# Kernel optimization log

Measured on AMD Instinct MI355X. Metric: run time of the kernel, lower is better.

Reference implementation:

```python
import jax, jax.numpy as jnp
import numpy as np

NUM_TAGS = 40
SEQ_LEN = 512
BATCH = 2048
INIT_W = 0.57735


def setup_inputs() -> dict:
    key = jax.random.key(0)
    k_em, k_tag, k_tr, k_st, k_en = jax.random.split(key, 5)
    emissions = jax.random.normal(k_em, (SEQ_LEN, BATCH, NUM_TAGS), dtype=jnp.float32)
    tags = jax.random.randint(k_tag, (SEQ_LEN, BATCH), 0, NUM_TAGS, dtype=jnp.int32)
    mask = jnp.ones((SEQ_LEN, BATCH), dtype=bool)
    transitions = jax.random.uniform(k_tr, (NUM_TAGS, NUM_TAGS), minval=-INIT_W, maxval=INIT_W, dtype=jnp.float32)
    start_transitions = jax.random.uniform(k_st, (NUM_TAGS,), minval=-INIT_W, maxval=INIT_W, dtype=jnp.float32)
    end_transitions = jax.random.uniform(k_en, (NUM_TAGS,), minval=-INIT_W, maxval=INIT_W, dtype=jnp.float32)
    return {
        'emissions': emissions,
        'tags': tags,
        'mask': mask,
        'transitions': transitions,
        'start_transitions': start_transitions,
        'end_transitions': end_transitions,
    }


def _seq_score(emissions, tags, mask, transitions, start_transitions, end_transitions):
    # emissions: (L,B,T), tags/mask: (L,B)
    L, B, T = emissions.shape
    maskf = mask.astype(emissions.dtype)
    # emission score of the gold tag at each step: (L,B)
    em = jnp.take_along_axis(emissions, tags[:, :, None].astype(jnp.int32), axis=2)[..., 0]
    score = start_transitions[tags[0]] + em[0]
    # transition + emission for steps 1..L-1, masked
    trans_step = transitions[tags[:-1], tags[1:]]  # (L-1,B)
    score = score + jnp.sum((trans_step + em[1:]) * maskf[1:], axis=0)
    seq_ends = jnp.sum(mask.astype(jnp.int32), axis=0) - 1  # (B,)
    last_tags = tags[seq_ends, jnp.arange(B)]
    score = score + end_transitions[last_tags]
    return score


def _log_normalizer(emissions, mask, transitions, start_transitions, end_transitions):
    # Forward algorithm: sequential scan over time with (B,T) state.
    score0 = start_transitions[None, :] + emissions[0]  # (B,T)

    def step(score, inp):
        em_t, m_t = inp  # (B,T), (B,)
        # broadcast: (B,T_prev,1) + (T_prev,T_next) + (B,1,T_next)
        next_score = jax.nn.logsumexp(score[:, :, None] + transitions[None, :, :] + em_t[:, None, :], axis=1)
        score = jnp.where(m_t[:, None], next_score, score)
        return score, None

    score, _ = jax.lax.scan(step, score0, (emissions[1:], mask[1:]))
    score = score + end_transitions[None, :]
    return jax.nn.logsumexp(score, axis=1)  # (B,)


def reference(emissions, tags, mask, transitions, start_transitions, end_transitions):
    log_num = _seq_score(emissions, tags, mask, transitions, start_transitions, end_transitions)
    log_den = _log_normalizer(emissions, mask, transitions, start_transitions, end_transitions)
    llh = log_num - log_den
    return jnp.sum(llh)  # reduction='sum'
```

## Files before the change

kernel.cpp:

```cpp
#include <hip/hip_runtime.h>

#define L   512
#define B   2048
#define NT  40

#define LOG2E 1.4426950408889634f
#define LN2   0.6931471805599453f

#define EXP2(x) __builtin_amdgcn_exp2f(x)
#define LOG2(x) __builtin_amdgcn_logf(x)

typedef float f32x4  __attribute__((ext_vector_type(4)));
typedef short bf16x8 __attribute__((ext_vector_type(8)));
typedef unsigned int uint4v __attribute__((ext_vector_type(4)));

#define MFMA(a, b, c) __builtin_amdgcn_mfma_f32_16x16x32_bf16(a, b, c, 0, 0, 0)

__device__ __forceinline__ unsigned short bf16_rtn(float x) {
    unsigned int u = __float_as_uint(x);
    u += 0x7FFFu + ((u >> 16) & 1u);
    return (unsigned short)(u >> 16);
}
__device__ __forceinline__ unsigned int cvtpk(float lo, float hi) {
    unsigned int r;
    asm("v_cvt_pk_bf16_f32 %0, %1, %2" : "=v"(r) : "v"(lo), "v"(hi));
    return r;
}
__device__ __forceinline__ float bf2f(short x) {
    return __int_as_float(((int)(unsigned short)x) << 16);
}
__device__ __forceinline__ float bperm_f(int addr, float v) {
    return __int_as_float(__builtin_amdgcn_ds_bpermute(addr, __float_as_int(v)));
}

extern "C" __global__ void __launch_bounds__(128, 2)
crf_main(const float* __restrict__ em, const int* __restrict__ tags,
         const float* __restrict__ trans, const float* __restrict__ st,
         const float* __restrict__ en, float* __restrict__ partial)
{
    __shared__ float sE[NT * NT];
    __shared__ float sT[NT * NT];
    __shared__ float sSt[NT];
    __shared__ float sEn[NT];
    __shared__ float sEn2[NT];
    __shared__ __align__(16) unsigned int sBi[2][16][28];
    __shared__ float sCB[16];
    __shared__ float sNB[16];

    const int tid = threadIdx.x;
    for (int k = tid; k < NT * NT; k += 128) {
        float v = trans[k];
        sT[k] = v;
        sE[k] = __expf(v);
    }
    if (tid < NT) { sSt[tid] = st[tid]; sEn[tid] = en[tid]; sEn2[tid] = en[tid] * LOG2E; }
    __syncthreads();

    const int wave = tid >> 6;
    const int lane = tid & 63;
    const int c    = lane & 15;
    const int g    = lane >> 4;
    const int bc   = blockIdx.x * 16 + c;
    const int i2   = 8 + ((g < 2) ? g : g - 2);
    const int i2s  = (g < 2) ? 32 + 4 * g : 0;
    const int an_addr = c * 4;

    unsigned int (*sBw)[28] = sBi[wave];

    bf16x8 Af[3][2];
#pragma unroll
    for (int mt = 0; mt < 3; ++mt) {
#pragma unroll
        for (int ks = 0; ks < 2; ++ks) {
            bf16x8 af;
#pragma unroll
            for (int e = 0; e < 8; ++e) {
                int k = 32 * ks + 8 * g + e;
                int m = 16 * mt + c;
                float v = 0.f;
                if (k < NT && m < NT)
                    v = (wave == 0) ? sE[k * NT + m] : sE[m * NT + k];
                af[e] = (short)bf16_rtn(v);
            }
            Af[mt][ks] = af;
        }
    }

    const size_t rs = (size_t)B * NT;
    const int* tgp = tags + bc;
    const size_t eb0 = (size_t)bc * NT;

    f32x4 P0, P1, P2;
    float Cf, numer;
    int   Cint = 0;
    int   tg_run;

    auto WRITEB = [&]() {
        uint2 W;
        W.x = cvtpk(P0[0], P0[1]); W.y = cvtpk(P0[2], P0[3]);
        *(uint2*)&sBw[c][2 * g] = W;
        W.x = cvtpk(P1[0], P1[1]); W.y = cvtpk(P1[2], P1[3]);
        *(uint2*)&sBw[c][8 + 2 * g] = W;
        W.x = cvtpk(P2[0], P2[1]); W.y = cvtpk(P2[2], P2[3]);
        *(uint2*)&sBw[c][16 + 2 * g] = W;
    };
    auto READ_MFMA = [&](f32x4& d0, f32x4& d1, f32x4& d2) {
        uint4v u0 = *(const uint4v*)&sBw[c][4 * g];
        uint4v u1 = *(const uint4v*)&sBw[c][16];
        bf16x8 b0 = __builtin_bit_cast(bf16x8, u0);
        bf16x8 b1 = __builtin_bit_cast(bf16x8, u1);
        f32x4 z = {0.f, 0.f, 0.f, 0.f};
        d0 = MFMA(Af[0][0], b0, z); d0 = MFMA(Af[0][1], b1, d0);
        d1 = MFMA(Af[1][0], b0, z); d1 = MFMA(Af[1][1], b1, d1);
        d2 = MFMA(Af[2][0], b0, z); d2 = MFMA(Af[2][1], b1, d2);
    };

#define LDFRAGS(d0, d1, d2, t) { \
        const f32x4* rp = (const f32x4*)(em + (size_t)(t) * rs + eb0); \
        d0 = rp[g]; d1 = rp[4 + g]; d2 = rp[i2]; }
#define MKX(X, F) { _Pragma("unroll") for (int r = 0; r < 4; ++r) X[r] = EXP2(F[r] * LOG2E); }

    if (wave == 0) {
        f32x4 F0, F1, F2;
        LDFRAGS(F0, F1, F2, 0);
#pragma unroll
        for (int r = 0; r < 4; ++r) {
            P0[r] = (sSt[4 * g + r] + F0[r]) * LOG2E;
            P1[r] = (sSt[16 + 4 * g + r] + F1[r]) * LOG2E;
            P2[r] = (sSt[i2s + r] + F2[r]) * LOG2E;
        }
        float m0 = bperm_f(an_addr, P0[0]);
        Cf = m0 + 6.f;
#pragma unroll
        for (int r = 0; r < 4; ++r) {
            P0[r] = EXP2(P0[r] - m0 - 6.f);
            P1[r] = EXP2(P1[r] - m0 - 6.f);
            P2[r] = (g < 2) ? EXP2(P2[r] - m0 - 6.f) : 0.f;
        }
        WRITEB();
        tg_run = tgp[0];
        numer = sSt[tg_run] + em[eb0 + tg_run];

        f32x4 FA0, FA1, FA2, FB0, FB1, FB2;
        LDFRAGS(FA0, FA1, FA2, 1); LDFRAGS(FB0, FB1, FB2, 2);
        int gA = tgp[(size_t)1 * B], gB = tgp[(size_t)2 * B];
        int g2A = tgp[(size_t)3 * B], g2B = tgp[(size_t)4 * B];
        float evA = em[(size_t)1 * rs + eb0 + gA];
        float evB = em[(size_t)2 * rs + eb0 + gB];

        for (int it = 0; it < 128; ++it) {
            const int t = 1 + 2 * it;
            int g3A = tgp[(size_t)(t + 4) * B];
            int g3B = tgp[(size_t)(t + 5) * B];
            float ev2A = em[(size_t)(t + 2) * rs + eb0 + g2A];
            float ev2B = em[(size_t)(t + 3) * rs + eb0 + g2B];
            f32x4 GA0, GA1, GA2, GB0, GB1, GB2;
            LDFRAGS(GA0, GA1, GA2, t + 2); LDFRAGS(GB0, GB1, GB2, t + 3);
            f32x4 XA0, XA1, XA2, XB0, XB1, XB2;
            MKX(XA0, FA0); MKX(XA1, FA1); MKX(XA2, FA2);
            MKX(XB0, FB0); MKX(XB1, FB1); MKX(XB2, FB2);
            f32x4 d0, d1, d2;
            READ_MFMA(d0, d1, d2);
#pragma unroll
            for (int r = 0; r < 4; ++r) {
                P0[r] = XA0[r] * d0[r];
                P1[r] = XA1[r] * d1[r];
                P2[r] = XA2[r] * d2[r];
            }
            float pendv = bperm_f(an_addr, P0[0]);
            WRITEB();
            numer += sT[tg_run * NT + gA] + evA; tg_run = gA;
            unsigned int pb = __float_as_uint(pendv);
            int e0 = (int)((pb >> 23) & 255u);
            float s = __uint_as_float((unsigned)(248 - e0) << 23);
            Cint += e0 - 121;
#pragma unroll
            for (int r = 0; r < 4; ++r) { XB0[r] *= s; XB1[r] *= s; XB2[r] *= s; }
            READ_MFMA(d0, d1, d2);
#pragma unroll
            for (int r = 0; r < 4; ++r) {
                P0[r] = XB0[r] * d0[r];
                P1[r] = XB1[r] * d1[r];
                P2[r] = XB2[r] * d2[r];
            }
            WRITEB();
            numer += sT[tg_run * NT + gB] + evB; tg_run = gB;
            FA0 = GA0; FA1 = GA1; FA2 = GA2; FB0 = GB0; FB1 = GB1; FB2 = GB2;
            gA = g2A; gB = g2B; g2A = g3A; g2B = g3B;
            evA = ev2A; evB = ev2B;
        }
    } else {
#pragma unroll
        for (int r = 0; r < 4; ++r) {
            P0[r] = EXP2(sEn2[4 * g + r] - sEn2[0] - 6.f);
            P1[r] = EXP2(sEn2[16 + 4 * g + r] - sEn2[0] - 6.f);
            P2[r] = (g < 2) ? EXP2(sEn2[i2s + r] - sEn2[0] - 6.f) : 0.f;
        }
        Cf = sEn2[0] + 6.f;
        tg_run = tgp[(size_t)511 * B];
        numer = sEn[tg_run];

        f32x4 FA0, FA1, FA2, FB0, FB1, FB2;
        LDFRAGS(FA0, FA1, FA2, 511); LDFRAGS(FB0, FB1, FB2, 510);
        int gA = tgp[(size_t)510 * B], gB = tgp[(size_t)509 * B];
        int g2A = tgp[(size_t)508 * B], g2B = tgp[(size_t)507 * B];
        float evA = em[(size_t)511 * rs + eb0 + tg_run];
        float evB = em[(size_t)510 * rs + eb0 + gA];

        for (int it = 0; it < 127; ++it) {
            const int t = 511 - 2 * it;
            int g3A = tgp[(size_t)(t - 5) * B];
            int g3B = tgp[(size_t)(t - 6) * B];
            float ev2A = em[(size_t)(t - 2) * rs + eb0 + gB];
            float ev2B = em[(size_t)(t - 3) * rs + eb0 + g2A];
            f32x4 GA0, GA1, GA2, GB0, GB1, GB2;
            LDFRAGS(GA0, GA1, GA2, t - 2); LDFRAGS(GB0, GB1, GB2, t - 3);
            f32x4 XA0, XA1, XA2, XB0, XB1, XB2;
            MKX(XA0, FA0); MKX(XA1, FA1); MKX(XA2, FA2);
            MKX(XB0, FB0); MKX(XB1, FB1); MKX(XB2, FB2);
#pragma unroll
            for (int r = 0; r < 4; ++r) { P0[r] *= XA0[r]; P1[r] *= XA1[r]; P2[r] *= XA2[r]; }
            float pendv = bperm_f(an_addr, P0[0]);
            WRITEB();
            f32x4 d0, d1, d2;
            READ_MFMA(d0, d1, d2);
            P0 = d0; P1 = d1; P2 = d2;
            numer += sT[gA * NT + tg_run] + evA; tg_run = gA;
            unsigned int pb = __float_as_uint(pendv);
            int e0 = (int)((pb >> 23) & 255u);
            float s = __uint_as_float((unsigned)(248 - e0) << 23);
            Cint += e0 - 121;
#pragma unroll
            for (int r = 0; r < 4; ++r) { XB0[r] *= s; XB1[r] *= s; XB2[r] *= s; }
#pragma unroll
            for (int r = 0; r < 4; ++r) { P0[r] *= XB0[r]; P1[r] *= XB1[r]; P2[r] *= XB2[r]; }
            WRITEB();
            READ_MFMA(d0, d1, d2);
            P0 = d0; P1 = d1; P2 = d2;
            numer += sT[gB * NT + tg_run] + evB; tg_run = gB;
            FA0 = GA0; FA1 = GA1; FA2 = GA2; FB0 = GB0; FB1 = GB1; FB2 = GB2;
            gA = g2A; gB = g2B; g2A = g3A; g2B = g3B;
            evA = ev2A; evB = ev2B;
        }
        {
            f32x4 XT0, XT1, XT2;
            MKX(XT0, FA0); MKX(XT1, FA1); MKX(XT2, FA2);
#pragma unroll
            for (int r = 0; r < 4; ++r) { P0[r] *= XT0[r]; P1[r] *= XT1[r]; P2[r] *= XT2[r]; }
            float a = bperm_f(an_addr, P0[0]);
            int e0 = (int)((__float_as_uint(a) >> 23) & 255u);
            float s = __uint_as_float((unsigned)(248 - e0) << 23);
            Cint += e0 - 121;
#pragma unroll
            for (int r = 0; r < 4; ++r) { P0[r] *= s; P1[r] *= s; P2[r] *= s; }
            WRITEB();
            f32x4 d0, d1, d2;
            READ_MFMA(d0, d1, d2);
            P0 = d0; P1 = d1; P2 = d2;
            numer += sT[gA * NT + tg_run] + evA; tg_run = gA;
        }
        {
            float a = bperm_f(an_addr, P0[0]);
            int e0 = (int)((__float_as_uint(a) >> 23) & 255u);
            float s = __uint_as_float((unsigned)(248 - e0) << 23);
            Cint += e0 - 121;
#pragma unroll
            for (int r = 0; r < 4; ++r) { P0[r] *= s; P1[r] *= s; P2[r] *= s; }
            WRITEB();
        }
        if (lane < 16) { sCB[lane] = Cf + (float)Cint; sNB[lane] = numer; }
    }

    __syncthreads();

    if (wave == 0) {
        float ps = 0.f;
        uint4v ua = *(const uint4v*)&sBi[0][c][4 * g];
        uint4v ub = *(const uint4v*)&sBi[1][c][4 * g];
        bf16x8 a0 = __builtin_bit_cast(bf16x8, ua);
        bf16x8 b0 = __builtin_bit_cast(bf16x8, ub);
#pragma unroll
        for (int e = 0; e < 8; ++e) ps += bf2f(a0[e]) * bf2f(b0[e]);
        if (g == 0) {
            uint4v uc = *(const uint4v*)&sBi[0][c][16];
            uint4v ud = *(const uint4v*)&sBi[1][c][16];
            bf16x8 a1 = __builtin_bit_cast(bf16x8, uc);
            bf16x8 b1 = __builtin_bit_cast(bf16x8, ud);
#pragma unroll
            for (int e = 0; e < 8; ++e) ps += bf2f(a1[e]) * bf2f(b1[e]);
        }
        ps += __shfl_xor(ps, 16, 64);
        ps += __shfl_xor(ps, 32, 64);
        if (lane < 16) {
            float den = LN2 * ((Cf + (float)Cint) + sCB[lane] + LOG2(ps));
            float llh = numer + sNB[lane] - den;
            llh += __shfl_xor(llh, 1, 64);
            llh += __shfl_xor(llh, 2, 64);
            llh += __shfl_xor(llh, 4, 64);
            llh += __shfl_xor(llh, 8, 64);
            if (lane == 0) partial[blockIdx.x] = llh;
        }
    }
}

extern "C" __global__ void __launch_bounds__(256)
crf_reduce(const float* __restrict__ partial, float* __restrict__ out, int n)
{
    const int tid = threadIdx.x;
    float s = 0.f;
    for (int i = tid; i < n; i += 256) s += partial[i];
#pragma unroll
    for (int off = 32; off; off >>= 1) s += __shfl_xor(s, off, 64);
    __shared__ float red[4];
    if ((tid & 63) == 0) red[tid >> 6] = s;
    __syncthreads();
    if (tid == 0) out[0] = red[0] + red[1] + red[2] + red[3];
}

extern "C" void kernel_launch(void* const* d_in, const int* in_sizes, int n_in,
                              void* d_out, int out_size, void* d_ws, size_t ws_size,
                              hipStream_t stream)
{
    const float* em   = (const float*)d_in[0];
    const int*   tags = (const int*)d_in[1];
    const float* tr   = (const float*)d_in[3];
    const float* st   = (const float*)d_in[4];
    const float* en   = (const float*)d_in[5];

    float* partial = (float*)d_ws;
    const int nblocks = B / 16;

    crf_main<<<nblocks, 128, 0, stream>>>(em, tags, tr, st, en, partial);
    crf_reduce<<<1, 256, 0, stream>>>(partial, (float*)d_out, nblocks);
}
```

Measured before the change: 86.66 us.

## Keep forward state in registers by permuting MFMA K layout, drop LDS round-trip

Reorders the K dimension of the transition-matrix A fragments so that each lane's own C-fragment outputs line up with the B-operand K slots it feeds to the next MFMA. The state vector can then be packed directly into bf16 registers instead of being written to and read back from LDS every time step. This removes an LDS store/load and its wait from the serial recurrence critical path. In exchange, the packing uses software bf16 rounding in place of the cvt_pk instruction, and the final state is written to LDS only once after the loop.

```diff
diff --git a/kernel.cpp b/kernel.cpp
--- a/kernel.cpp
+++ b/kernel.cpp
@@ -20,6 +20,9 @@
     unsigned int u = __float_as_uint(x);
     u += 0x7FFFu + ((u >> 16) & 1u);
     return (unsigned short)(u >> 16);
+}
+__device__ __forceinline__ unsigned int pk2(float lo, float hi) {
+    return (unsigned int)bf16_rtn(lo) | ((unsigned int)bf16_rtn(hi) << 16);
 }
 __device__ __forceinline__ unsigned int cvtpk(float lo, float hi) {
     unsigned int r;
@@ -75,11 +78,13 @@
             bf16x8 af;
 #pragma unroll
             for (int e = 0; e < 8; ++e) {
-                int k = 32 * ks + 8 * g + e;
+                int tag;
+                if (ks == 0) tag = (e < 4) ? (4 * g + e) : (16 + 4 * g + (e - 4));
+                else         tag = (g < 2 && e < 4) ? (32 + 4 * g + e) : -1;
                 int m = 16 * mt + c;
                 float v = 0.f;
-                if (k < NT && m < NT)
-                    v = (wave == 0) ? sE[k * NT + m] : sE[m * NT + k];
+                if (tag >= 0 && m < NT)
+                    v = (wave == 0) ? sE[tag * NT + m] : sE[m * NT + tag];
                 af[e] = (short)bf16_rtn(v);
             }
             Af[mt][ks] = af;
@@ -91,10 +96,27 @@
     const size_t eb0 = (size_t)bc * NT;
 
     f32x4 P0, P1, P2;
+    bf16x8 u0, u1;
     float Cf, numer;
     int   Cint = 0;
     int   tg_run;
 
+    auto PACK = [&]() {
+        uint4v w0;
+        w0[0] = pk2(P0[0], P0[1]); w0[1] = pk2(P0[2], P0[3]);
+        w0[2] = pk2(P1[0], P1[1]); w0[3] = pk2(P1[2], P1[3]);
+        u0 = __builtin_bit_cast(bf16x8, w0);
+        uint4v w1;
+        w1[0] = pk2(P2[0], P2[1]); w1[1] = pk2(P2[2], P2[3]);
+        w1[2] = 0u; w1[3] = 0u;
+        u1 = __builtin_bit_cast(bf16x8, w1);
+    };
+    auto MSTEP = [&](f32x4& d0, f32x4& d1, f32x4& d2) {
+        f32x4 z = {0.f, 0.f, 0.f, 0.f};
+        d0 = MFMA(Af[0][0], u0, z); d0 = MFMA(Af[0][1], u1, d0);
+        d1 = MFMA(Af[1][0], u0, z); d1 = MFMA(Af[1][1], u1, d1);
+        d2 = MFMA(Af[2][0], u0, z); d2 = MFMA(Af[2][1], u1, d2);
+    };
     auto WRITEB = [&]() {
         uint2 W;
         W.x = cvtpk(P0[0], P0[1]); W.y = cvtpk(P0[2], P0[3]);
@@ -104,16 +126,6 @@
         W.x = cvtpk(P2[0], P2[1]); W.y = cvtpk(P2[2], P2[3]);
         *(uint2*)&sBw[c][16 + 2 * g] = W;
     };
-    auto READ_MFMA = [&](f32x4& d0, f32x4& d1, f32x4& d2) {
-        uint4v u0 = *(const uint4v*)&sBw[c][4 * g];
-        uint4v u1 = *(const uint4v*)&sBw[c][16];
-        bf16x8 b0 = __builtin_bit_cast(bf16x8, u0);
-        bf16x8 b1 = __builtin_bit_cast(bf16x8, u1);
-        f32x4 z = {0.f, 0.f, 0.f, 0.f};
-        d0 = MFMA(Af[0][0], b0, z); d0 = MFMA(Af[0][1], b1, d0);
-        d1 = MFMA(Af[1][0], b0, z); d1 = MFMA(Af[1][1], b1, d1);
-        d2 = MFMA(Af[2][0], b0, z); d2 = MFMA(Af[2][1], b1, d2);
-    };
 
 #define LDFRAGS(d0, d1, d2, t) { \
         const f32x4* rp = (const f32x4*)(em + (size_t)(t) * rs + eb0); \
@@ -137,7 +149,7 @@
             P1[r] = EXP2(P1[r] - m0 - 6.f);
             P2[r] = (g < 2) ? EXP2(P2[r] - m0 - 6.f) : 0.f;
         }
-        WRITEB();
+        PACK();
         tg_run = tgp[0];
         numer = sSt[tg_run] + em[eb0 + tg_run];
 
@@ -160,7 +172,7 @@
             MKX(XA0, FA0); MKX(XA1, FA1); MKX(XA2, FA2);
             MKX(XB0, FB0); MKX(XB1, FB1); MKX(XB2, FB2);
             f32x4 d0, d1, d2;
-            READ_MFMA(d0, d1, d2);
+            MSTEP(d0, d1, d2);
 #pragma unroll
             for (int r = 0; r < 4; ++r) {
                 P0[r] = XA0[r] * d0[r];
@@ -168,7 +180,7 @@
                 P2[r] = XA2[r] * d2[r];
             }
             float pendv = bperm_f(an_addr, P0[0]);
-            WRITEB();
+            PACK();
             numer += sT[tg_run * NT + gA] + evA; tg_run = gA;
             unsigned int pb = __float_as_uint(pendv);
             int e0 = (int)((pb >> 23) & 255u);
@@ -176,19 +188,20 @@
             Cint += e0 - 121;
 #pragma unroll
             for (int r = 0; r < 4; ++r) { XB0[r] *= s; XB1[r] *= s; XB2[r] *= s; }
-            READ_MFMA(d0, d1, d2);
+            MSTEP(d0, d1, d2);
 #pragma unroll
             for (int r = 0; r < 4; ++r) {
                 P0[r] = XB0[r] * d0[r];
                 P1[r] = XB1[r] * d1[r];
                 P2[r] = XB2[r] * d2[r];
             }
-            WRITEB();
+            PACK();
             numer += sT[tg_run * NT + gB] + evB; tg_run = gB;
             FA0 = GA0; FA1 = GA1; FA2 = GA2; FB0 = GB0; FB1 = GB1; FB2 = GB2;
             gA = g2A; gB = g2B; g2A = g3A; g2B = g3B;
             evA = ev2A; evB = ev2B;
         }
+        WRITEB();
     } else {
 #pragma unroll
         for (int r = 0; r < 4; ++r) {
@@ -221,9 +234,9 @@
 #pragma unroll
             for (int r = 0; r < 4; ++r) { P0[r] *= XA0[r]; P1[r] *= XA1[r]; P2[r] *= XA2[r]; }
             float pendv = bperm_f(an_addr, P0[0]);
-            WRITEB();
+            PACK();
             f32x4 d0, d1, d2;
-            READ_MFMA(d0, d1, d2);
+            MSTEP(d0, d1, d2);
             P0 = d0; P1 = d1; P2 = d2;
             numer += sT[gA * NT + tg_run] + evA; tg_run = gA;
             unsigned int pb = __float_as_uint(pendv);
@@ -234,8 +247,8 @@
             for (int r = 0; r < 4; ++r) { XB0[r] *= s; XB1[r] *= s; XB2[r] *= s; }
 #pragma unroll
             for (int r = 0; r < 4; ++r) { P0[r] *= XB0[r]; P1[r] *= XB1[r]; P2[r] *= XB2[r]; }
-            WRITEB();
-            READ_MFMA(d0, d1, d2);
+            PACK();
+            MSTEP(d0, d1, d2);
             P0 = d0; P1 = d1; P2 = d2;
             numer += sT[gB * NT + tg_run] + evB; tg_run = gB;
             FA0 = GA0; FA1 = GA1; FA2 = GA2; FB0 = GB0; FB1 = GB1; FB2 = GB2;
@@ -253,9 +266,9 @@
             Cint += e0 - 121;
 #pragma unroll
             for (int r = 0; r < 4; ++r) { P0[r] *= s; P1[r] *= s; P2[r] *= s; }
-            WRITEB();
+            PACK();
             f32x4 d0, d1, d2;
-            READ_MFMA(d0, d1, d2);
+            MSTEP(d0, d1, d2);
             P0 = d0; P1 = d1; P2 = d2;
             numer += sT[gA * NT + tg_run] + evA; tg_run = gA;
         }
```

Result: slower. 106.5 us (+22.9%).
